# Kernel optimization log

Hardware: AMD Instinct MI355X
Metric: run time of the kernel (lower is better)

Reference implementation:

```python
import jax, jax.numpy as jnp
import numpy as np

B, N, D, H = 2, 2048, 1024, 16
HD = D // H  # head_dim = 64


def setup_inputs() -> dict:
    key = jax.random.key(0)
    ks = jax.random.split(key, 11)
    s = 1.0 / np.sqrt(D)
    return {
        "query": jax.random.normal(ks[0], (B, N, D), jnp.float32),
        "key": jax.random.normal(ks[1], (B, N, D), jnp.float32),
        "value": jax.random.normal(ks[2], (B, N, D), jnp.float32),
        # nn.Linear params: y = x @ W.T + b, W is [out, in]
        "Wq": jax.random.uniform(ks[3], (D, D), jnp.float32, -s, s),
        "bq": jax.random.uniform(ks[4], (D,), jnp.float32, -s, s),
        "Wk": jax.random.uniform(ks[5], (D, D), jnp.float32, -s, s),
        "bk": jax.random.uniform(ks[6], (D,), jnp.float32, -s, s),
        "Wv": jax.random.uniform(ks[7], (D, D), jnp.float32, -s, s),
        "bv": jax.random.uniform(ks[8], (D,), jnp.float32, -s, s),
        "Wo": jax.random.uniform(ks[9], (D, D), jnp.float32, -s, s),
        "bo": jax.random.uniform(ks[10], (D,), jnp.float32, -s, s),
    }


def reference(query, key, value, Wq, bq, Wk, bk, Wv, bv, Wo, bo):
    # QKV projections, split into heads: [B, H, N, HD]
    Q = (query @ Wq.T + bq).reshape(B, N, H, HD).transpose(0, 2, 1, 3)
    K = (key @ Wk.T + bk).reshape(B, N, H, HD).transpose(0, 2, 1, 3)
    V = (value @ Wv.T + bv).reshape(B, N, H, HD).transpose(0, 2, 1, 3)
    # scaled dot-product attention with explicit A: [B, H, N, N]
    scale = 1.0 / jnp.sqrt(jnp.float32(HD))
    A = jax.nn.softmax(jnp.einsum('bhid,bhjd->bhij', Q, K) * scale, axis=-1)
    Vh = jnp.einsum('bhij,bhjd->bhid', A, V)  # [B, H, N, HD]
    V_ = Vh.transpose(0, 2, 1, 3).reshape(B, N, D)
    out = V_ @ Wo.T + bo
    return (out, A)
```

## Files before the change

kernel.cpp:

```cpp
#include <hip/hip_runtime.h>
#include <hip/hip_bf16.h>
#include <cstdint>
#include <cstddef>
#include <type_traits>

#define B_  2
#define N_  2048
#define D_  1024
#define H_  16
#define HD_ 64
#define M_  (B_*N_)

typedef __bf16 bf16_t;
typedef bf16_t bf16x8 __attribute__((ext_vector_type(8)));
typedef bf16_t bf16x4 __attribute__((ext_vector_type(4)));
typedef float  f32x4  __attribute__((ext_vector_type(4)));

static_assert(sizeof(bf16x8) == 16, "bf16x8 must be 16B");

__device__ __forceinline__ f32x4 mfma_bf16(bf16x8 a, bf16x8 b, f32x4 c) {
    return __builtin_amdgcn_mfma_f32_16x16x32_bf16(a, b, c, 0, 0, 0);
}

template <typename TX, typename TY>
__global__ __launch_bounds__(256) void proj(const TX* __restrict__ X,
                                            const float* __restrict__ W,
                                            const float* __restrict__ bias,
                                            TY* __restrict__ Y,
                                            int N, int K)
{
    __shared__ __align__(16) bf16_t Xs[64 * 72];
    __shared__ __align__(16) bf16_t Ws[64 * 72];
    const int tid  = threadIdx.x;
    const int wave = tid >> 6;
    const int lane = tid & 63;
    const int l16  = lane & 15;
    const int q    = lane >> 4;
    const int m0   = blockIdx.y * 64;
    const int n0   = blockIdx.x * 64;

    f32x4 acc[4] = {};

    for (int k0 = 0; k0 < K; k0 += 64) {
        __syncthreads();
        if constexpr (std::is_same_v<TX, float>) {
            #pragma unroll
            for (int p = 0; p < 4; p++) {
                int c    = p * 256 + tid;
                int row  = c >> 4;
                int col4 = (c & 15) * 4;
                f32x4 v = *(const f32x4*)&X[(size_t)(m0 + row) * K + k0 + col4];
                bf16x4 o;
                #pragma unroll
                for (int e = 0; e < 4; e++) o[e] = (bf16_t)v[e];
                *(bf16x4*)&Xs[row * 72 + col4] = o;
            }
        } else {
            #pragma unroll
            for (int p = 0; p < 2; p++) {
                int c   = p * 256 + tid;
                int row = c >> 3;
                int col = (c & 7) * 8;
                *(bf16x8*)&Xs[row * 72 + col] =
                    *(const bf16x8*)&X[(size_t)(m0 + row) * K + k0 + col];
            }
        }
        #pragma unroll
        for (int p = 0; p < 4; p++) {
            int c    = p * 256 + tid;
            int row  = c >> 4;
            int col4 = (c & 15) * 4;
            f32x4 v = *(const f32x4*)&W[(size_t)(n0 + row) * K + k0 + col4];
            bf16x4 o;
            #pragma unroll
            for (int e = 0; e < 4; e++) o[e] = (bf16_t)v[e];
            *(bf16x4*)&Ws[row * 72 + col4] = o;
        }
        __syncthreads();
        #pragma unroll
        for (int ks = 0; ks < 64; ks += 32) {
            bf16x8 a = *(const bf16x8*)&Xs[(wave * 16 + l16) * 72 + ks + q * 8];
            #pragma unroll
            for (int nt = 0; nt < 4; nt++) {
                bf16x8 b = *(const bf16x8*)&Ws[(nt * 16 + l16) * 72 + ks + q * 8];
                acc[nt] = mfma_bf16(a, b, acc[nt]);
            }
        }
    }

    #pragma unroll
    for (int nt = 0; nt < 4; nt++) {
        int colg = n0 + nt * 16 + l16;
        float bv = bias[colg];
        #pragma unroll
        for (int reg = 0; reg < 4; reg++) {
            int rowg = m0 + wave * 16 + q * 4 + reg;
            Y[(size_t)rowg * N + colg] = (TY)(acc[nt][reg] + bv);
        }
    }
}

__global__ __launch_bounds__(256) void qk_rowsum(const bf16_t* __restrict__ Q,
                                                 const bf16_t* __restrict__ Km,
                                                 float* __restrict__ rinv)
{
    const int tid  = threadIdx.x;
    const int wave = tid >> 6;
    const int lane = tid & 63;
    const int l16  = lane & 15;
    const int q    = lane >> 4;
    const int bh   = blockIdx.y;
    const int b    = bh >> 4;
    const int h    = bh & 15;
    const int i0   = blockIdx.x * 64;

    const bf16_t* Qp = Q + (size_t)(b * N_ + i0 + wave * 16 + l16) * D_ + h * HD_ + q * 8;
    bf16x8 a0 = *(const bf16x8*)(Qp);
    bf16x8 a1 = *(const bf16x8*)(Qp + 32);

    const float scale = 0.125f;
    float rs[4] = {0.f, 0.f, 0.f, 0.f};

    for (int j0 = 0; j0 < N_; j0 += 128) {
        #pragma unroll
        for (int nt = 0; nt < 8; nt++) {
            const bf16_t* Kp = Km + (size_t)(b * N_ + j0 + nt * 16 + l16) * D_ + h * HD_ + q * 8;
            bf16x8 b0 = *(const bf16x8*)(Kp);
            bf16x8 b1 = *(const bf16x8*)(Kp + 32);
            f32x4 c = {};
            c = mfma_bf16(a0, b0, c);
            c = mfma_bf16(a1, b1, c);
            #pragma unroll
            for (int reg = 0; reg < 4; reg++) rs[reg] += __expf(c[reg] * scale);
        }
    }

    #pragma unroll
    for (int reg = 0; reg < 4; reg++) {
        float v = rs[reg];
        v += __shfl_xor(v, 1);
        v += __shfl_xor(v, 2);
        v += __shfl_xor(v, 4);
        v += __shfl_xor(v, 8);
        if (l16 == 0) {
            int rowg = i0 + wave * 16 + q * 4 + reg;
            rinv[bh * N_ + rowg] = 1.0f / v;
        }
    }
}

__global__ __launch_bounds__(256) void qk_av(const bf16_t* __restrict__ Q,
                                             const bf16_t* __restrict__ Km,
                                             const bf16_t* __restrict__ V,
                                             const float* __restrict__ rinv,
                                             float* __restrict__ A,
                                             bf16_t* __restrict__ Vh)
{
    __shared__ __align__(16) bf16_t Vt[64 * 72];
    __shared__ __align__(16) bf16_t Ps[64 * 72];
    const int tid  = threadIdx.x;
    const int wave = tid >> 6;
    const int lane = tid & 63;
    const int l16  = lane & 15;
    const int q    = lane >> 4;
    const int bh   = blockIdx.y;
    const int b    = bh >> 4;
    const int h    = bh & 15;
    const int i0   = blockIdx.x * 64;

    const bf16_t* Qp = Q + (size_t)(b * N_ + i0 + wave * 16 + l16) * D_ + h * HD_ + q * 8;
    bf16x8 a0 = *(const bf16x8*)(Qp);
    bf16x8 a1 = *(const bf16x8*)(Qp + 32);

    float rv[4];
    #pragma unroll
    for (int reg = 0; reg < 4; reg++)
        rv[reg] = rinv[bh * N_ + i0 + wave * 16 + q * 4 + reg];

    float* Ab = A + ((size_t)bh << 22);
    const float scale = 0.125f;
    f32x4 acco[4] = {};

    for (int j0 = 0; j0 < N_; j0 += 64) {
        __syncthreads();
        #pragma unroll
        for (int p = 0; p < 2; p++) {
            int c  = p * 256 + tid;
            int jr = c >> 3;
            int hc = (c & 7) * 8;
            bf16x8 v = *(const bf16x8*)&V[(size_t)(b * N_ + j0 + jr) * D_ + h * HD_ + hc];
            #pragma unroll
            for (int e = 0; e < 8; e++) Vt[(hc + e) * 72 + jr] = v[e];
        }
        #pragma unroll
        for (int nt = 0; nt < 4; nt++) {
            const bf16_t* Kp = Km + (size_t)(b * N_ + j0 + nt * 16 + l16) * D_ + h * HD_ + q * 8;
            bf16x8 b0 = *(const bf16x8*)(Kp);
            bf16x8 b1 = *(const bf16x8*)(Kp + 32);
            f32x4 c = {};
            c = mfma_bf16(a0, b0, c);
            c = mfma_bf16(a1, b1, c);
            #pragma unroll
            for (int reg = 0; reg < 4; reg++) {
                float p = __expf(c[reg] * scale) * rv[reg];
                int rowl = wave * 16 + q * 4 + reg;
                int colg = j0 + nt * 16 + l16;
                __builtin_nontemporal_store(p, &Ab[(size_t)(i0 + rowl) * N_ + colg]);
                Ps[rowl * 72 + nt * 16 + l16] = (bf16_t)p;
            }
        }
        __syncthreads();
        #pragma unroll
        for (int ks = 0; ks < 64; ks += 32) {
            bf16x8 a = *(const bf16x8*)&Ps[(wave * 16 + l16) * 72 + ks + q * 8];
            #pragma unroll
            for (int nt = 0; nt < 4; nt++) {
                bf16x8 bfr = *(const bf16x8*)&Vt[(nt * 16 + l16) * 72 + ks + q * 8];
                acco[nt] = mfma_bf16(a, bfr, acco[nt]);
            }
        }
    }

    #pragma unroll
    for (int nt = 0; nt < 4; nt++) {
        int colg = h * HD_ + nt * 16 + l16;
        #pragma unroll
        for (int reg = 0; reg < 4; reg++) {
            int rowg = i0 + wave * 16 + q * 4 + reg;
            Vh[(size_t)(b * N_ + rowg) * D_ + colg] = (bf16_t)acco[nt][reg];
        }
    }
}

extern "C" void kernel_launch(void* const* d_in, const int* in_sizes, int n_in,
                              void* d_out, int out_size, void* d_ws, size_t ws_size,
                              hipStream_t stream)
{
    const float* query = (const float*)d_in[0];
    const float* key   = (const float*)d_in[1];
    const float* value = (const float*)d_in[2];
    const float* Wq = (const float*)d_in[3];
    const float* bq = (const float*)d_in[4];
    const float* Wk = (const float*)d_in[5];
    const float* bk = (const float*)d_in[6];
    const float* Wv = (const float*)d_in[7];
    const float* bv = (const float*)d_in[8];
    const float* Wo = (const float*)d_in[9];
    const float* bo = (const float*)d_in[10];

    float* out  = (float*)d_out;
    float* Aout = out + (size_t)B_ * N_ * D_;

    char* ws = (char*)d_ws;
    bf16_t* Qw   = (bf16_t*)(ws);
    bf16_t* Kw   = (bf16_t*)(ws + (size_t)8  * 1024 * 1024);
    bf16_t* Vw   = (bf16_t*)(ws + (size_t)16 * 1024 * 1024);
    bf16_t* Vhw  = (bf16_t*)(ws + (size_t)24 * 1024 * 1024);
    float*  rinv = (float*) (ws + (size_t)32 * 1024 * 1024);

    dim3 blk(256);

    dim3 gproj(D_ / 64, M_ / 64);
    proj<float, bf16_t><<<gproj, blk, 0, stream>>>(query, Wq, bq, Qw, D_, D_);
    proj<float, bf16_t><<<gproj, blk, 0, stream>>>(key,   Wk, bk, Kw, D_, D_);
    proj<float, bf16_t><<<gproj, blk, 0, stream>>>(value, Wv, bv, Vw, D_, D_);

    dim3 grs(N_ / 64, B_ * H_);
    qk_rowsum<<<grs, blk, 0, stream>>>(Qw, Kw, rinv);

    dim3 gqa(N_ / 64, B_ * H_);
    qk_av<<<gqa, blk, 0, stream>>>(Qw, Kw, Vw, rinv, Aout, Vhw);

    proj<bf16_t, float><<<gproj, blk, 0, stream>>>(Vhw, Wo, bo, out, D_, D_);
}
```

Before: 1.035 ms.

## Pre-convert inputs to bf16, use LDS DMA loads, fuse rowsum into attention, coalesce A stores

A new kernel converts the activations and the Q/K/V weights to bf16 once, using the tail of the A output buffer as scratch. Projections then load tiles with global_load_lds DMA instead of converting in registers. The rowsum pass is merged into the attention kernel, removing one launch and the rinv buffer. The probabilities are staged in fp32 LDS so A is written with coalesced 16-byte nontemporal stores. This relies on the A scratch region being overwritten later by the attention kernel, and the separate conversion pass adds extra traffic.

After: 882.3 us. 14.7% less time.

```diff
diff --git a/kernel.cpp b/kernel.cpp
--- a/kernel.cpp
+++ b/kernel.cpp
@@ -22,15 +22,48 @@
     return __builtin_amdgcn_mfma_f32_16x16x32_bf16(a, b, c, 0, 0, 0);
 }
 
-template <typename TX, typename TY>
-__global__ __launch_bounds__(256) void proj(const TX* __restrict__ X,
-                                            const float* __restrict__ W,
-                                            const float* __restrict__ bias,
-                                            TY* __restrict__ Y,
-                                            int N, int K)
-{
-    __shared__ __align__(16) bf16_t Xs[64 * 72];
+__device__ __forceinline__ void gload_lds16(const bf16_t* g, bf16_t* l) {
+    __builtin_amdgcn_global_load_lds(
+        (const __attribute__((address_space(1))) uint32_t*)(const void*)g,
+        (__attribute__((address_space(3))) uint32_t*)(void*)l,
+        16, 0, 0);
+}
+
+__global__ __launch_bounds__(256) void cvt6(
+    const float* __restrict__ s0, const float* __restrict__ s1, const float* __restrict__ s2,
+    const float* __restrict__ s3, const float* __restrict__ s4, const float* __restrict__ s5,
+    bf16_t* __restrict__ d0, bf16_t* __restrict__ d1, bf16_t* __restrict__ d2,
+    bf16_t* __restrict__ d3, bf16_t* __restrict__ d4, bf16_t* __restrict__ d5)
+{
+    const float* src; bf16_t* dst; int n8;
+    switch (blockIdx.y) {
+        case 0:  src = s0; dst = d0; n8 = (M_*D_)/8; break;
+        case 1:  src = s1; dst = d1; n8 = (M_*D_)/8; break;
+        case 2:  src = s2; dst = d2; n8 = (M_*D_)/8; break;
+        case 3:  src = s3; dst = d3; n8 = (D_*D_)/8; break;
+        case 4:  src = s4; dst = d4; n8 = (D_*D_)/8; break;
+        default: src = s5; dst = d5; n8 = (D_*D_)/8; break;
+    }
+    int c = blockIdx.x * 256 + threadIdx.x;
+    if (c >= n8) return;
+    const f32x4* sp = (const f32x4*)(src + (size_t)c * 8);
+    f32x4 v0 = sp[0], v1 = sp[1];
+    bf16x8 o;
+    #pragma unroll
+    for (int e = 0; e < 4; e++) { o[e] = (bf16_t)v0[e]; o[e + 4] = (bf16_t)v1[e]; }
+    *(bf16x8*)(dst + (size_t)c * 8) = o;
+}
+
+template <bool WBF16, typename TY>
+__global__ __launch_bounds__(256) void projb(const bf16_t* __restrict__ X,
+                                             const void* __restrict__ Wp,
+                                             const float* __restrict__ bias,
+                                             TY* __restrict__ Y,
+                                             int N, int K)
+{
+    __shared__ __align__(16) bf16_t Xs[64 * 64];
     __shared__ __align__(16) bf16_t Ws[64 * 72];
+    constexpr int WP = WBF16 ? 64 : 72;
     const int tid  = threadIdx.x;
     const int wave = tid >> 6;
     const int lane = tid & 63;
@@ -43,46 +76,41 @@
 
     for (int k0 = 0; k0 < K; k0 += 64) {
         __syncthreads();
-        if constexpr (std::is_same_v<TX, float>) {
+        #pragma unroll
+        for (int i = 0; i < 2; i++) {
+            int g = wave * 128 + i * 64 + lane;
+            gload_lds16(&X[(size_t)(m0 + (g >> 3)) * K + k0 + (lane & 7) * 8],
+                        &Xs[(wave * 128 + i * 64) * 8]);
+        }
+        if constexpr (WBF16) {
+            const bf16_t* Wb = (const bf16_t*)Wp;
+            #pragma unroll
+            for (int i = 0; i < 2; i++) {
+                int g = wave * 128 + i * 64 + lane;
+                gload_lds16(&Wb[(size_t)(n0 + (g >> 3)) * K + k0 + (lane & 7) * 8],
+                            &Ws[(wave * 128 + i * 64) * 8]);
+            }
+        } else {
+            const float* Wf = (const float*)Wp;
             #pragma unroll
             for (int p = 0; p < 4; p++) {
                 int c    = p * 256 + tid;
                 int row  = c >> 4;
                 int col4 = (c & 15) * 4;
-                f32x4 v = *(const f32x4*)&X[(size_t)(m0 + row) * K + k0 + col4];
+                f32x4 v = *(const f32x4*)&Wf[(size_t)(n0 + row) * K + k0 + col4];
                 bf16x4 o;
                 #pragma unroll
                 for (int e = 0; e < 4; e++) o[e] = (bf16_t)v[e];
-                *(bf16x4*)&Xs[row * 72 + col4] = o;
-            }
-        } else {
-            #pragma unroll
-            for (int p = 0; p < 2; p++) {
-                int c   = p * 256 + tid;
-                int row = c >> 3;
-                int col = (c & 7) * 8;
-                *(bf16x8*)&Xs[row * 72 + col] =
-                    *(const bf16x8*)&X[(size_t)(m0 + row) * K + k0 + col];
-            }
-        }
-        #pragma unroll
-        for (int p = 0; p < 4; p++) {
-            int c    = p * 256 + tid;
-            int row  = c >> 4;
-            int col4 = (c & 15) * 4;
-            f32x4 v = *(const f32x4*)&W[(size_t)(n0 + row) * K + k0 + col4];
-            bf16x4 o;
-            #pragma unroll
-            for (int e = 0; e < 4; e++) o[e] = (bf16_t)v[e];
-            *(bf16x4*)&Ws[row * 72 + col4] = o;
+                *(bf16x4*)&Ws[row * 72 + col4] = o;
+            }
         }
         __syncthreads();
         #pragma unroll
         for (int ks = 0; ks < 64; ks += 32) {
-            bf16x8 a = *(const bf16x8*)&Xs[(wave * 16 + l16) * 72 + ks + q * 8];
+            bf16x8 a = *(const bf16x8*)&Xs[(wave * 16 + l16) * 64 + ks + q * 8];
             #pragma unroll
             for (int nt = 0; nt < 4; nt++) {
-                bf16x8 b = *(const bf16x8*)&Ws[(nt * 16 + l16) * 72 + ks + q * 8];
+                bf16x8 b = *(const bf16x8*)&Ws[(nt * 16 + l16) * WP + ks + q * 8];
                 acc[nt] = mfma_bf16(a, b, acc[nt]);
             }
         }
@@ -100,10 +128,14 @@
     }
 }
 
-__global__ __launch_bounds__(256) void qk_rowsum(const bf16_t* __restrict__ Q,
-                                                 const bf16_t* __restrict__ Km,
-                                                 float* __restrict__ rinv)
-{
+__global__ __launch_bounds__(256) void qk_av_fused(const bf16_t* __restrict__ Q,
+                                                   const bf16_t* __restrict__ Km,
+                                                   const bf16_t* __restrict__ V,
+                                                   float* __restrict__ A,
+                                                   bf16_t* __restrict__ Vh)
+{
+    __shared__ __align__(16) bf16_t Vt[64 * 72];
+    __shared__ __align__(16) float  Pf[64 * 68];
     const int tid  = threadIdx.x;
     const int wave = tid >> 6;
     const int lane = tid & 63;
@@ -119,8 +151,8 @@
     bf16x8 a1 = *(const bf16x8*)(Qp + 32);
 
     const float scale = 0.125f;
+
     float rs[4] = {0.f, 0.f, 0.f, 0.f};
-
     for (int j0 = 0; j0 < N_; j0 += 128) {
         #pragma unroll
         for (int nt = 0; nt < 8; nt++) {
@@ -134,7 +166,7 @@
             for (int reg = 0; reg < 4; reg++) rs[reg] += __expf(c[reg] * scale);
         }
     }
-
+    float rv[4];
     #pragma unroll
     for (int reg = 0; reg < 4; reg++) {
         float v = rs[reg];
@@ -142,43 +174,10 @@
         v += __shfl_xor(v, 2);
         v += __shfl_xor(v, 4);
         v += __shfl_xor(v, 8);
-        if (l16 == 0) {
-            int rowg = i0 + wave * 16 + q * 4 + reg;
-            rinv[bh * N_ + rowg] = 1.0f / v;
-        }
-    }
-}
-
-__global__ __launch_bounds__(256) void qk_av(const bf16_t* __restrict__ Q,
-                                             const bf16_t* __restrict__ Km,
-                                             const bf16_t* __restrict__ V,
-                                             const float* __restrict__ rinv,
-                                             float* __restrict__ A,
-                                             bf16_t* __restrict__ Vh)
-{
-    __shared__ __align__(16) bf16_t Vt[64 * 72];
-    __shared__ __align__(16) bf16_t Ps[64 * 72];
-    const int tid  = threadIdx.x;
-    const int wave = tid >> 6;
-    const int lane = tid & 63;
-    const int l16  = lane & 15;
-    const int q    = lane >> 4;
-    const int bh   = blockIdx.y;
-    const int b    = bh >> 4;
-    const int h    = bh & 15;
-    const int i0   = blockIdx.x * 64;
-
-    const bf16_t* Qp = Q + (size_t)(b * N_ + i0 + wave * 16 + l16) * D_ + h * HD_ + q * 8;
-    bf16x8 a0 = *(const bf16x8*)(Qp);
-    bf16x8 a1 = *(const bf16x8*)(Qp + 32);
-
-    float rv[4];
-    #pragma unroll
-    for (int reg = 0; reg < 4; reg++)
-        rv[reg] = rinv[bh * N_ + i0 + wave * 16 + q * 4 + reg];
+        rv[reg] = 1.0f / v;
+    }
 
     float* Ab = A + ((size_t)bh << 22);
-    const float scale = 0.125f;
     f32x4 acco[4] = {};
 
     for (int j0 = 0; j0 < N_; j0 += 64) {
@@ -203,16 +202,25 @@
             #pragma unroll
             for (int reg = 0; reg < 4; reg++) {
                 float p = __expf(c[reg] * scale) * rv[reg];
-                int rowl = wave * 16 + q * 4 + reg;
-                int colg = j0 + nt * 16 + l16;
-                __builtin_nontemporal_store(p, &Ab[(size_t)(i0 + rowl) * N_ + colg]);
-                Ps[rowl * 72 + nt * 16 + l16] = (bf16_t)p;
-            }
-        }
-        __syncthreads();
+                Pf[(wave * 16 + q * 4 + reg) * 68 + nt * 16 + l16] = p;
+            }
+        }
+        __syncthreads();
+        #pragma unroll
+        for (int k = 0; k < 4; k++) {
+            int row  = k * 16 + (tid >> 4);
+            int col4 = (tid & 15) * 4;
+            f32x4 v = *(const f32x4*)&Pf[row * 68 + col4];
+            __builtin_nontemporal_store(v, (f32x4*)&Ab[(size_t)(i0 + row) * N_ + j0 + col4]);
+        }
         #pragma unroll
         for (int ks = 0; ks < 64; ks += 32) {
-            bf16x8 a = *(const bf16x8*)&Ps[(wave * 16 + l16) * 72 + ks + q * 8];
+            const float* pp = &Pf[(wave * 16 + l16) * 68 + ks + q * 8];
+            f32x4 p0 = *(const f32x4*)(pp);
+            f32x4 p1 = *(const f32x4*)(pp + 4);
+            bf16x8 a;
+            #pragma unroll
+            for (int e = 0; e < 4; e++) { a[e] = (bf16_t)p0[e]; a[e + 4] = (bf16_t)p1[e]; }
             #pragma unroll
             for (int nt = 0; nt < 4; nt++) {
                 bf16x8 bfr = *(const bf16x8*)&Vt[(nt * 16 + l16) * 72 + ks + q * 8];
@@ -251,25 +259,32 @@
     float* out  = (float*)d_out;
     float* Aout = out + (size_t)B_ * N_ * D_;
 
+    char* scr = (char*)Aout + ((size_t)536870912 - (size_t)32 * 1024 * 1024);
+    bf16_t* qb  = (bf16_t*)(scr);
+    bf16_t* kb  = (bf16_t*)(scr + (size_t)8  * 1024 * 1024);
+    bf16_t* vb  = (bf16_t*)(scr + (size_t)16 * 1024 * 1024);
+    bf16_t* Wqb = (bf16_t*)(scr + (size_t)24 * 1024 * 1024);
+    bf16_t* Wkb = (bf16_t*)(scr + (size_t)26 * 1024 * 1024);
+    bf16_t* Wvb = (bf16_t*)(scr + (size_t)28 * 1024 * 1024);
+
     char* ws = (char*)d_ws;
     bf16_t* Qw   = (bf16_t*)(ws);
     bf16_t* Kw   = (bf16_t*)(ws + (size_t)8  * 1024 * 1024);
     bf16_t* Vw   = (bf16_t*)(ws + (size_t)16 * 1024 * 1024);
     bf16_t* Vhw  = (bf16_t*)(ws + (size_t)24 * 1024 * 1024);
-    float*  rinv = (float*) (ws + (size_t)32 * 1024 * 1024);
 
     dim3 blk(256);
 
+    cvt6<<<dim3(2048, 6), blk, 0, stream>>>(query, key, value, Wq, Wk, Wv,
+                                            qb, kb, vb, Wqb, Wkb, Wvb);
+
     dim3 gproj(D_ / 64, M_ / 64);
-    proj<float, bf16_t><<<gproj, blk, 0, stream>>>(query, Wq, bq, Qw, D_, D_);
-    proj<float, bf16_t><<<gproj, blk, 0, stream>>>(key,   Wk, bk, Kw, D_, D_);
-    proj<float, bf16_t><<<gproj, blk, 0, stream>>>(value, Wv, bv, Vw, D_, D_);
-
-    dim3 grs(N_ / 64, B_ * H_);
-    qk_rowsum<<<grs, blk, 0, stream>>>(Qw, Kw, rinv);
+    projb<true,  bf16_t><<<gproj, blk, 0, stream>>>(qb, Wqb, bq, Qw, D_, D_);
+    projb<true,  bf16_t><<<gproj, blk, 0, stream>>>(kb, Wkb, bk, Kw, D_, D_);
+    projb<true,  bf16_t><<<gproj, blk, 0, stream>>>(vb, Wvb, bv, Vw, D_, D_);
 
     dim3 gqa(N_ / 64, B_ * H_);
-    qk_av<<<gqa, blk, 0, stream>>>(Qw, Kw, Vw, rinv, Aout, Vhw);
-
-    proj<bf16_t, float><<<gproj, blk, 0, stream>>>(Vhw, Wo, bo, out, D_, D_);
-}
+    qk_av_fused<<<gqa, blk, 0, stream>>>(Qw, Kw, Vw, Aout, Vhw);
+
+    projb<false, float><<<gproj, blk, 0, stream>>>(Vhw, Wo, bo, out, D_, D_);
+}
```
